# Optimization experiments

Measured on AMD Instinct MI355X. Metric: run time of the kernel, lower is better.

## Reference

```python
import math
import jax, jax.numpy as jnp
import numpy as np

L, B, T, D = 16, 2, 2048, 1024

def setup_inputs() -> dict:
    key = jax.random.key(0)
    ks = jax.random.split(key, 6)
    return {
        "layer_outputs": jax.random.normal(ks[0], (L, B, T, D), jnp.float32),
        # nn.Linear weights, init std=0.02 (torch Linear computes x @ W^T)
        "w_q": jax.random.normal(ks[1], (D, D), jnp.float32) * 0.02,
        "w_k": jax.random.normal(ks[2], (D, D), jnp.float32) * 0.02,
        # per-layer LayerScalingFactor scalars, init 1/L (jittered so grads are nontrivial)
        "ca_scales": 1.0 / L + jax.random.normal(ks[3], (L,), jnp.float32) * 0.01,
        # CrossLayerAttention temperature, init 1.0
        "ca_temp": jnp.ones((1,), jnp.float32),
        # output LayerNorm affine params
        "ln_w": jnp.ones((D,), jnp.float32) + jax.random.normal(ks[4], (D,), jnp.float32) * 0.01,
        "ln_b": jax.random.normal(ks[5], (D,), jnp.float32) * 0.01,
    }

def reference(layer_outputs, w_q, w_k, ca_scales, ca_temp, ln_w, ln_b):
    # AllLayerXSA.aggregate_layers, aggregation_mode='attention', num_heads=1 (H=1, so H*D == head_dim)
    l, b, t, d = layer_outputs.shape
    current = layer_outputs[-1]                                    # query = last layer, [B,T,D]
    q = jnp.einsum('btd,ed->bte', current, w_q)                    # query_proj (no bias)
    k = jnp.einsum('lbtd,ed->lbte', layer_outputs, w_k)            # key_proj over stacked layers
    # per-token scores over layers: [B,T,L]
    scores = jnp.einsum('btd,lbtd->btl', q, k) / (math.sqrt(d) * jnp.abs(ca_temp))
    attn = jax.nn.softmax(scores, axis=-1)
    # per-layer scaling + renormalization
    attn = attn * ca_scales                                        # broadcast over L
    attn = attn / (jnp.sum(attn, axis=-1, keepdims=True) + 1e-6)
    # accumulate: output += scale_l * attn_w_l * layer_l (scale applied a second time, as in source)
    out = jnp.einsum('btl,l,lbtd->btd', attn, ca_scales, layer_outputs)
    # output LayerNorm(head_dim), torch default eps=1e-5, biased variance
    mean = jnp.mean(out, axis=-1, keepdims=True)
    var = jnp.mean(jnp.square(out - mean), axis=-1, keepdims=True)
    out = (out - mean) / jnp.sqrt(var + 1e-5) * ln_w + ln_b
    return out
```

## Files before the change

### kernel.cpp

```cpp
#include <hip/hip_runtime.h>
#include <hip/hip_bf16.h>

#define LNUM 16
#define DDIM 1024
#define MTOK 4096

using bf16x8 = __attribute__((ext_vector_type(8))) short;
using s4v    = __attribute__((ext_vector_type(4))) short;
using f32x4  = __attribute__((ext_vector_type(4))) float;

__device__ inline short f2b(float f) {
  __hip_bfloat16 h = __float2bfloat16(f);
  union { __hip_bfloat16 h; short s; } u; u.h = h; return u.s;
}
__device__ inline float b2f(short s) {
  unsigned int u = ((unsigned int)(unsigned short)s) << 16;
  float f; __builtin_memcpy(&f, &u, 4); return f;
}
__device__ inline float bitsf(unsigned int u) {
  float f; __builtin_memcpy(&f, &u, 4); return f;
}

__global__ __launch_bounds__(256)
void pre_k(const float* __restrict__ wk, const float* __restrict__ wq,
           short* __restrict__ Wt,
           const float* __restrict__ xlast, short* __restrict__ xb)
{
  __shared__ short As[2][64 * 64];
  __shared__ short Bs[2][64 * 64];
  const int tid = threadIdx.x;

  if (blockIdx.x >= 256) {
    const size_t i = ((size_t)(blockIdx.x - 256) * 256 + tid) * 8;
    const float4 a = *reinterpret_cast<const float4*>(xlast + i);
    const float4 b = *reinterpret_cast<const float4*>(xlast + i + 4);
    bf16x8 v = { f2b(a.x), f2b(a.y), f2b(a.z), f2b(a.w),
                 f2b(b.x), f2b(b.y), f2b(b.z), f2b(b.w) };
    *reinterpret_cast<bf16x8*>(xb + i) = v;
    return;
  }

  const int lane = tid & 63;
  const int wave = tid >> 6;
  const int m0 = (blockIdx.x & 15) * 64;
  const int n0 = (blockIdx.x >> 4) * 64;
  const int wm = (wave >> 1) * 32;
  const int wn = (wave & 1) * 32;

  f32x4 acc[2][2] = {};
  const int col = tid & 63;
  const int kg  = tid >> 6;

  float ar[16], br[16];
  auto load = [&](int k0) {
    #pragma unroll
    for (int j = 0; j < 16; ++j) {
      const size_t k = (size_t)(k0 + kg * 16 + j);
      ar[j] = wk[k * 1024 + m0 + col];
      br[j] = wq[k * 1024 + n0 + col];
    }
  };
  auto store_lds = [&](int buf) {
    bf16x8 va0 = { f2b(ar[0]), f2b(ar[1]), f2b(ar[2]), f2b(ar[3]),
                   f2b(ar[4]), f2b(ar[5]), f2b(ar[6]), f2b(ar[7]) };
    bf16x8 va1 = { f2b(ar[8]), f2b(ar[9]), f2b(ar[10]), f2b(ar[11]),
                   f2b(ar[12]), f2b(ar[13]), f2b(ar[14]), f2b(ar[15]) };
    bf16x8 vb0 = { f2b(br[0]), f2b(br[1]), f2b(br[2]), f2b(br[3]),
                   f2b(br[4]), f2b(br[5]), f2b(br[6]), f2b(br[7]) };
    bf16x8 vb1 = { f2b(br[8]), f2b(br[9]), f2b(br[10]), f2b(br[11]),
                   f2b(br[12]), f2b(br[13]), f2b(br[14]), f2b(br[15]) };
    const int sw = (col & 7) << 4;
    const int b0 = (col * 128 + kg * 32) ^ sw;
    const int b1 = (col * 128 + kg * 32 + 16) ^ sw;
    char* pa = (char*)&As[buf][0];
    char* pb = (char*)&Bs[buf][0];
    *reinterpret_cast<bf16x8*>(pa + b0) = va0;
    *reinterpret_cast<bf16x8*>(pa + b1) = va1;
    *reinterpret_cast<bf16x8*>(pb + b0) = vb0;
    *reinterpret_cast<bf16x8*>(pb + b1) = vb1;
  };

  const int rl = lane & 15;
  const int hi = lane >> 4;
  auto compute = [&](int buf) {
    #pragma unroll
    for (int kk = 0; kk < 2; ++kk) {
      bf16x8 af[2], bfv[2];
      #pragma unroll
      for (int f = 0; f < 2; ++f) {
        const int row = wm + f * 16 + rl;
        af[f] = *reinterpret_cast<const bf16x8*>(
            (const char*)&As[buf][0] + ((row * 128 + kk * 64 + hi * 16) ^ ((row & 7) << 4)));
      }
      #pragma unroll
      for (int g = 0; g < 2; ++g) {
        const int row = wn + g * 16 + rl;
        bfv[g] = *reinterpret_cast<const bf16x8*>(
            (const char*)&Bs[buf][0] + ((row * 128 + kk * 64 + hi * 16) ^ ((row & 7) << 4)));
      }
      #pragma unroll
      for (int f = 0; f < 2; ++f)
        #pragma unroll
        for (int g = 0; g < 2; ++g)
          acc[f][g] = __builtin_amdgcn_mfma_f32_16x16x32_bf16(af[f], bfv[g], acc[f][g], 0, 0, 0);
    }
  };

  load(0);
  for (int t = 0; t < 16; ++t) {
    store_lds(t & 1);
    if (t < 15) load((t + 1) * 64);
    __syncthreads();
    compute(t & 1);
  }

  const int cl = lane & 15;
  const int rb = (lane >> 4) * 4;
  #pragma unroll
  for (int f = 0; f < 2; ++f)
    #pragma unroll
    for (int g = 0; g < 2; ++g) {
      size_t c = (size_t)(n0 + wn + g * 16 + cl);
      #pragma unroll
      for (int r = 0; r < 4; ++r) {
        size_t rr = (size_t)(m0 + wm + f * 16 + rb + r);
        Wt[rr * 1024 + c] = f2b(acc[f][g][r]);
      }
    }
}

__global__ __launch_bounds__(512)
void qk_gemm_k(const short* __restrict__ A, const short* __restrict__ B,
               short* __restrict__ C)
{
  __shared__ short As[2][128 * 64];
  __shared__ short Bs[2][128 * 64];
  const int tid  = threadIdx.x;
  const int lane = tid & 63;
  const int wave = tid >> 6;
  const int m0 = blockIdx.x * 128;
  const int n0 = blockIdx.y * 128;
  const int wm = (wave >> 2) * 64;
  const int wn = (wave & 3) * 32;

  f32x4 acc[4][2] = {};

  const int srow = lane >> 3;
  const int swz  = ((lane & 7) * 16) ^ (srow << 4);

  auto stage = [&](int buf, int k0) {
    #pragma unroll
    for (int c = 0; c < 2; ++c) {
      const int ch = wave * 2 + c;
      const int r  = ch * 8 + srow;
      const short* ga = A + (size_t)(m0 + r) * 1024 + k0 + (swz >> 1);
      __builtin_amdgcn_global_load_lds(
          (const __attribute__((address_space(1))) void*)ga,
          (__attribute__((address_space(3))) void*)&As[buf][ch * 512], 16, 0, 0);
      const short* gb = B + (size_t)(n0 + r) * 1024 + k0 + (swz >> 1);
      __builtin_amdgcn_global_load_lds(
          (const __attribute__((address_space(1))) void*)gb,
          (__attribute__((address_space(3))) void*)&Bs[buf][ch * 512], 16, 0, 0);
    }
  };

  const int rl = lane & 15;
  const int hi = lane >> 4;
  auto compute = [&](int buf) {
    #pragma unroll
    for (int kk = 0; kk < 2; ++kk) {
      bf16x8 af[4], bfv[2];
      #pragma unroll
      for (int i = 0; i < 4; ++i) {
        const int row = wm + i * 16 + rl;
        af[i] = *reinterpret_cast<const bf16x8*>(
            (const char*)&As[buf][0] + ((row * 128 + kk * 64 + hi * 16) ^ ((row & 7) << 4)));
      }
      #pragma unroll
      for (int g = 0; g < 2; ++g) {
        const int row = wn + g * 16 + rl;
        bfv[g] = *reinterpret_cast<const bf16x8*>(
            (const char*)&Bs[buf][0] + ((row * 128 + kk * 64 + hi * 16) ^ ((row & 7) << 4)));
      }
      #pragma unroll
      for (int i = 0; i < 4; ++i)
        #pragma unroll
        for (int g = 0; g < 2; ++g)
          acc[i][g] = __builtin_amdgcn_mfma_f32_16x16x32_bf16(af[i], bfv[g], acc[i][g], 0, 0, 0);
    }
  };

  stage(0, 0);
  __syncthreads();
  int buf = 0;
  for (int t = 0; t < 16; ++t) {
    if (t < 15) stage(buf ^ 1, (t + 1) * 64);
    compute(buf);
    __syncthreads();
    buf ^= 1;
  }

  const int cl = lane & 15;
  const int rb = (lane >> 4) * 4;
  #pragma unroll
  for (int i = 0; i < 4; ++i)
    #pragma unroll
    for (int g = 0; g < 2; ++g) {
      size_t c = (size_t)(n0 + wn + g * 16 + cl);
      #pragma unroll
      for (int r = 0; r < 4; ++r) {
        size_t rr = (size_t)(m0 + wm + i * 16 + rb + r);
        C[rr * 1024 + c] = f2b(acc[i][g][r]);
      }
    }
}

__global__ __launch_bounds__(256)
void fused_k(const float* __restrict__ layers, const short* __restrict__ qk,
             const float* __restrict__ scales, const float* __restrict__ temp,
             const float* __restrict__ lnw, const float* __restrict__ lnb,
             float* __restrict__ out)
{
  const int p    = blockIdx.x;
  const int tid  = threadIdx.x;
  const int lane = tid & 63;
  const int wave = tid >> 6;

  __shared__ float s_scales[16];
  __shared__ float s_red[4][16];
  __shared__ float s_scores[16];
  __shared__ float s_mv[4][2];

  if (tid < 16) s_scales[tid] = scales[tid];

  const size_t base = (size_t)p * DDIM + (size_t)tid * 4;
  s4v qv = *reinterpret_cast<const s4v*>(qk + base);
  const float q0 = b2f(qv.x), q1 = b2f(qv.y), q2 = b2f(qv.z), q3 = b2f(qv.w);

  unsigned int xpA[16], xpB[16];
  float v[16];
  #pragma unroll
  for (int l = 0; l < 16; ++l) {
    const float4 xv = *reinterpret_cast<const float4*>(layers + (size_t)l * MTOK * DDIM + base);
    v[l] = q0 * xv.x + q1 * xv.y + q2 * xv.z + q3 * xv.w;
    xpA[l] = ((unsigned int)(unsigned short)f2b(xv.y) << 16) | (unsigned short)f2b(xv.x);
    xpB[l] = ((unsigned int)(unsigned short)f2b(xv.w) << 16) | (unsigned short)f2b(xv.z);
  }

  #pragma unroll
  for (int j = 0; j < 8; ++j) {
    const bool hi = (lane & 1);
    float send = hi ? v[j] : v[j + 8];
    float keep = hi ? v[j + 8] : v[j];
    v[j] = keep + __shfl_xor(send, 1, 64);
  }
  #pragma unroll
  for (int j = 0; j < 4; ++j) {
    const bool hi = (lane & 2);
    float send = hi ? v[j] : v[j + 4];
    float keep = hi ? v[j + 4] : v[j];
    v[j] = keep + __shfl_xor(send, 2, 64);
  }
  #pragma unroll
  for (int j = 0; j < 2; ++j) {
    const bool hi = (lane & 4);
    float send = hi ? v[j] : v[j + 2];
    float keep = hi ? v[j + 2] : v[j];
    v[j] = keep + __shfl_xor(send, 4, 64);
  }
  {
    const bool hi = (lane & 8);
    float send = hi ? v[0] : v[1];
    float keep = hi ? v[1] : v[0];
    v[0] = keep + __shfl_xor(send, 8, 64);
  }
  v[0] += __shfl_xor(v[0], 16, 64);
  v[0] += __shfl_xor(v[0], 32, 64);
  if (lane < 16) {
    int l = ((lane & 1) << 3) | ((lane & 2) << 1) | ((lane & 4) >> 1) | ((lane & 8) >> 3);
    s_red[wave][l] = v[0];
  }
  __syncthreads();
  if (tid < 16)
    s_scores[tid] = s_red[0][tid] + s_red[1][tid] + s_red[2][tid] + s_red[3][tid];
  __syncthreads();

  const float inv = 1.0f / (32.0f * fabsf(temp[0]));
  float sc[16];
  float mx = -1e30f;
  #pragma unroll
  for (int l = 0; l < 16; ++l) { sc[l] = s_scores[l] * inv; mx = fmaxf(mx, sc[l]); }
  float se = 0.f;
  #pragma unroll
  for (int l = 0; l < 16; ++l) { sc[l] = __expf(sc[l] - mx); se += sc[l]; }
  const float rse = 1.0f / se;
  float t2 = 0.f;
  #pragma unroll
  for (int l = 0; l < 16; ++l) { sc[l] = sc[l] * rse * s_scales[l]; t2 += sc[l]; }
  const float rden = 1.0f / (t2 + 1e-6f);
  #pragma unroll
  for (int l = 0; l < 16; ++l) sc[l] *= s_scales[l] * rden;

  float o0 = 0.f, o1 = 0.f, o2 = 0.f, o3 = 0.f;
  #pragma unroll
  for (int l = 0; l < 16; ++l) {
    const float c = sc[l];
    o0 += c * bitsf(xpA[l] << 16);
    o1 += c * bitsf(xpA[l] & 0xffff0000u);
    o2 += c * bitsf(xpB[l] << 16);
    o3 += c * bitsf(xpB[l] & 0xffff0000u);
  }

  float sm = o0 + o1 + o2 + o3;
  float sq = o0 * o0 + o1 * o1 + o2 * o2 + o3 * o3;
  #pragma unroll
  for (int off = 1; off < 64; off <<= 1) {
    sm += __shfl_xor(sm, off, 64);
    sq += __shfl_xor(sq, off, 64);
  }
  if (lane == 0) { s_mv[wave][0] = sm; s_mv[wave][1] = sq; }
  __syncthreads();
  const float tsm = s_mv[0][0] + s_mv[1][0] + s_mv[2][0] + s_mv[3][0];
  const float tsq = s_mv[0][1] + s_mv[1][1] + s_mv[2][1] + s_mv[3][1];
  const float mean = tsm * (1.0f / 1024.0f);
  const float varv = tsq * (1.0f / 1024.0f) - mean * mean;
  const float rstd = rsqrtf(varv + 1e-5f);

  const float4 lw = *reinterpret_cast<const float4*>(lnw + (size_t)tid * 4);
  const float4 lb = *reinterpret_cast<const float4*>(lnb + (size_t)tid * 4);
  float4 res;
  res.x = (o0 - mean) * rstd * lw.x + lb.x;
  res.y = (o1 - mean) * rstd * lw.y + lb.y;
  res.z = (o2 - mean) * rstd * lw.z + lb.z;
  res.w = (o3 - mean) * rstd * lw.w + lb.w;
  *reinterpret_cast<float4*>(out + base) = res;
}

extern "C" void kernel_launch(void* const* d_in, const int* in_sizes, int n_in,
                              void* d_out, int out_size, void* d_ws, size_t ws_size,
                              hipStream_t stream)
{
  const float* layers = (const float*)d_in[0];
  const float* wq     = (const float*)d_in[1];
  const float* wk     = (const float*)d_in[2];
  const float* scales = (const float*)d_in[3];
  const float* temp   = (const float*)d_in[4];
  const float* lnw    = (const float*)d_in[5];
  const float* lnb    = (const float*)d_in[6];
  float* out = (float*)d_out;

  short* xb_ws = (short*)d_ws;
  short* wt_ws = xb_ws + (size_t)MTOK * DDIM;
  short* qk_ws = wt_ws + (size_t)DDIM * DDIM;

  const float* xlast = layers + (size_t)(LNUM - 1) * MTOK * DDIM;

  pre_k<<<dim3(256 + MTOK * DDIM / 2048), dim3(256), 0, stream>>>(wk, wq, wt_ws, xlast, xb_ws);
  qk_gemm_k<<<dim3(32, 8), dim3(512), 0, stream>>>(xb_ws, wt_ws, qk_ws);
  fused_k<<<dim3(MTOK), dim3(256), 0, stream>>>(layers, qk_ws, scales, temp, lnw, lnb, out);
}
```

Before: 92.80 us.

## Merge three kernels into one persistent kernel with software grid barriers

Replaces the weight-product, QK GEMM and fused attention/LayerNorm kernels with one 256-block persistent kernel that runs each phase in turn, separated by atomic-counter grid barriers. The x_last bf16 conversion is folded into the weight-GEMM phase, and the final phase processes 16 tokens per block, two at a time. This removes launch gaps and tail effects between kernels. In exchange it adds a hipMemsetAsync, spin-wait barriers that assume all 256 blocks are co-resident, and fewer resident threads for the memory-bound final phase, which may reduce latency hiding.

```diff
diff --git a/kernel.cpp b/kernel.cpp
--- a/kernel.cpp
+++ b/kernel.cpp
@@ -4,6 +4,7 @@
 #define LNUM 16
 #define DDIM 1024
 #define MTOK 4096
+#define NBLK 256
 
 using bf16x8 = __attribute__((ext_vector_type(8))) short;
 using s4v    = __attribute__((ext_vector_type(4))) short;
@@ -21,319 +22,321 @@
   float f; __builtin_memcpy(&f, &u, 4); return f;
 }
 
-__global__ __launch_bounds__(256)
-void pre_k(const float* __restrict__ wk, const float* __restrict__ wq,
-           short* __restrict__ Wt,
-           const float* __restrict__ xlast, short* __restrict__ xb)
-{
-  __shared__ short As[2][64 * 64];
-  __shared__ short Bs[2][64 * 64];
-  const int tid = threadIdx.x;
-
-  if (blockIdx.x >= 256) {
-    const size_t i = ((size_t)(blockIdx.x - 256) * 256 + tid) * 8;
-    const float4 a = *reinterpret_cast<const float4*>(xlast + i);
-    const float4 b = *reinterpret_cast<const float4*>(xlast + i + 4);
-    bf16x8 v = { f2b(a.x), f2b(a.y), f2b(a.z), f2b(a.w),
-                 f2b(b.x), f2b(b.y), f2b(b.z), f2b(b.w) };
-    *reinterpret_cast<bf16x8*>(xb + i) = v;
-    return;
-  }
-
-  const int lane = tid & 63;
-  const int wave = tid >> 6;
-  const int m0 = (blockIdx.x & 15) * 64;
-  const int n0 = (blockIdx.x >> 4) * 64;
-  const int wm = (wave >> 1) * 32;
-  const int wn = (wave & 1) * 32;
-
-  f32x4 acc[2][2] = {};
-  const int col = tid & 63;
-  const int kg  = tid >> 6;
-
-  float ar[16], br[16];
-  auto load = [&](int k0) {
-    #pragma unroll
-    for (int j = 0; j < 16; ++j) {
-      const size_t k = (size_t)(k0 + kg * 16 + j);
-      ar[j] = wk[k * 1024 + m0 + col];
-      br[j] = wq[k * 1024 + n0 + col];
-    }
-  };
-  auto store_lds = [&](int buf) {
-    bf16x8 va0 = { f2b(ar[0]), f2b(ar[1]), f2b(ar[2]), f2b(ar[3]),
-                   f2b(ar[4]), f2b(ar[5]), f2b(ar[6]), f2b(ar[7]) };
-    bf16x8 va1 = { f2b(ar[8]), f2b(ar[9]), f2b(ar[10]), f2b(ar[11]),
-                   f2b(ar[12]), f2b(ar[13]), f2b(ar[14]), f2b(ar[15]) };
-    bf16x8 vb0 = { f2b(br[0]), f2b(br[1]), f2b(br[2]), f2b(br[3]),
-                   f2b(br[4]), f2b(br[5]), f2b(br[6]), f2b(br[7]) };
-    bf16x8 vb1 = { f2b(br[8]), f2b(br[9]), f2b(br[10]), f2b(br[11]),
-                   f2b(br[12]), f2b(br[13]), f2b(br[14]), f2b(br[15]) };
-    const int sw = (col & 7) << 4;
-    const int b0 = (col * 128 + kg * 32) ^ sw;
-    const int b1 = (col * 128 + kg * 32 + 16) ^ sw;
-    char* pa = (char*)&As[buf][0];
-    char* pb = (char*)&Bs[buf][0];
-    *reinterpret_cast<bf16x8*>(pa + b0) = va0;
-    *reinterpret_cast<bf16x8*>(pa + b1) = va1;
-    *reinterpret_cast<bf16x8*>(pb + b0) = vb0;
-    *reinterpret_cast<bf16x8*>(pb + b1) = vb1;
-  };
-
-  const int rl = lane & 15;
-  const int hi = lane >> 4;
-  auto compute = [&](int buf) {
-    #pragma unroll
-    for (int kk = 0; kk < 2; ++kk) {
-      bf16x8 af[2], bfv[2];
-      #pragma unroll
-      for (int f = 0; f < 2; ++f) {
-        const int row = wm + f * 16 + rl;
-        af[f] = *reinterpret_cast<const bf16x8*>(
-            (const char*)&As[buf][0] + ((row * 128 + kk * 64 + hi * 16) ^ ((row & 7) << 4)));
-      }
-      #pragma unroll
-      for (int g = 0; g < 2; ++g) {
-        const int row = wn + g * 16 + rl;
-        bfv[g] = *reinterpret_cast<const bf16x8*>(
-            (const char*)&Bs[buf][0] + ((row * 128 + kk * 64 + hi * 16) ^ ((row & 7) << 4)));
-      }
-      #pragma unroll
-      for (int f = 0; f < 2; ++f)
-        #pragma unroll
-        for (int g = 0; g < 2; ++g)
-          acc[f][g] = __builtin_amdgcn_mfma_f32_16x16x32_bf16(af[f], bfv[g], acc[f][g], 0, 0, 0);
-    }
-  };
-
-  load(0);
-  for (int t = 0; t < 16; ++t) {
-    store_lds(t & 1);
-    if (t < 15) load((t + 1) * 64);
-    __syncthreads();
-    compute(t & 1);
-  }
-
-  const int cl = lane & 15;
-  const int rb = (lane >> 4) * 4;
-  #pragma unroll
-  for (int f = 0; f < 2; ++f)
-    #pragma unroll
-    for (int g = 0; g < 2; ++g) {
-      size_t c = (size_t)(n0 + wn + g * 16 + cl);
-      #pragma unroll
-      for (int r = 0; r < 4; ++r) {
-        size_t rr = (size_t)(m0 + wm + f * 16 + rb + r);
-        Wt[rr * 1024 + c] = f2b(acc[f][g][r]);
-      }
-    }
-}
-
-__global__ __launch_bounds__(512)
-void qk_gemm_k(const short* __restrict__ A, const short* __restrict__ B,
-               short* __restrict__ C)
-{
-  __shared__ short As[2][128 * 64];
-  __shared__ short Bs[2][128 * 64];
-  const int tid  = threadIdx.x;
-  const int lane = tid & 63;
-  const int wave = tid >> 6;
-  const int m0 = blockIdx.x * 128;
-  const int n0 = blockIdx.y * 128;
-  const int wm = (wave >> 2) * 64;
-  const int wn = (wave & 3) * 32;
-
-  f32x4 acc[4][2] = {};
-
-  const int srow = lane >> 3;
-  const int swz  = ((lane & 7) * 16) ^ (srow << 4);
-
-  auto stage = [&](int buf, int k0) {
-    #pragma unroll
-    for (int c = 0; c < 2; ++c) {
-      const int ch = wave * 2 + c;
-      const int r  = ch * 8 + srow;
-      const short* ga = A + (size_t)(m0 + r) * 1024 + k0 + (swz >> 1);
-      __builtin_amdgcn_global_load_lds(
-          (const __attribute__((address_space(1))) void*)ga,
-          (__attribute__((address_space(3))) void*)&As[buf][ch * 512], 16, 0, 0);
-      const short* gb = B + (size_t)(n0 + r) * 1024 + k0 + (swz >> 1);
-      __builtin_amdgcn_global_load_lds(
-          (const __attribute__((address_space(1))) void*)gb,
-          (__attribute__((address_space(3))) void*)&Bs[buf][ch * 512], 16, 0, 0);
-    }
-  };
-
-  const int rl = lane & 15;
-  const int hi = lane >> 4;
-  auto compute = [&](int buf) {
-    #pragma unroll
-    for (int kk = 0; kk < 2; ++kk) {
-      bf16x8 af[4], bfv[2];
-      #pragma unroll
-      for (int i = 0; i < 4; ++i) {
-        const int row = wm + i * 16 + rl;
-        af[i] = *reinterpret_cast<const bf16x8*>(
-            (const char*)&As[buf][0] + ((row * 128 + kk * 64 + hi * 16) ^ ((row & 7) << 4)));
-      }
-      #pragma unroll
-      for (int g = 0; g < 2; ++g) {
-        const int row = wn + g * 16 + rl;
-        bfv[g] = *reinterpret_cast<const bf16x8*>(
-            (const char*)&Bs[buf][0] + ((row * 128 + kk * 64 + hi * 16) ^ ((row & 7) << 4)));
-      }
-      #pragma unroll
-      for (int i = 0; i < 4; ++i)
-        #pragma unroll
-        for (int g = 0; g < 2; ++g)
-          acc[i][g] = __builtin_amdgcn_mfma_f32_16x16x32_bf16(af[i], bfv[g], acc[i][g], 0, 0, 0);
-    }
-  };
-
-  stage(0, 0);
+__device__ inline void grid_barrier(unsigned int* cnt) {
   __syncthreads();
-  int buf = 0;
-  for (int t = 0; t < 16; ++t) {
-    if (t < 15) stage(buf ^ 1, (t + 1) * 64);
-    compute(buf);
-    __syncthreads();
-    buf ^= 1;
-  }
-
-  const int cl = lane & 15;
-  const int rb = (lane >> 4) * 4;
-  #pragma unroll
-  for (int i = 0; i < 4; ++i)
-    #pragma unroll
-    for (int g = 0; g < 2; ++g) {
-      size_t c = (size_t)(n0 + wn + g * 16 + cl);
-      #pragma unroll
-      for (int r = 0; r < 4; ++r) {
-        size_t rr = (size_t)(m0 + wm + i * 16 + rb + r);
-        C[rr * 1024 + c] = f2b(acc[i][g][r]);
-      }
-    }
-}
-
-__global__ __launch_bounds__(256)
-void fused_k(const float* __restrict__ layers, const short* __restrict__ qk,
-             const float* __restrict__ scales, const float* __restrict__ temp,
-             const float* __restrict__ lnw, const float* __restrict__ lnb,
-             float* __restrict__ out)
-{
-  const int p    = blockIdx.x;
-  const int tid  = threadIdx.x;
-  const int lane = tid & 63;
-  const int wave = tid >> 6;
-
-  __shared__ float s_scales[16];
-  __shared__ float s_red[4][16];
-  __shared__ float s_scores[16];
-  __shared__ float s_mv[4][2];
-
-  if (tid < 16) s_scales[tid] = scales[tid];
-
-  const size_t base = (size_t)p * DDIM + (size_t)tid * 4;
-  s4v qv = *reinterpret_cast<const s4v*>(qk + base);
-  const float q0 = b2f(qv.x), q1 = b2f(qv.y), q2 = b2f(qv.z), q3 = b2f(qv.w);
-
-  unsigned int xpA[16], xpB[16];
-  float v[16];
-  #pragma unroll
-  for (int l = 0; l < 16; ++l) {
-    const float4 xv = *reinterpret_cast<const float4*>(layers + (size_t)l * MTOK * DDIM + base);
-    v[l] = q0 * xv.x + q1 * xv.y + q2 * xv.z + q3 * xv.w;
-    xpA[l] = ((unsigned int)(unsigned short)f2b(xv.y) << 16) | (unsigned short)f2b(xv.x);
-    xpB[l] = ((unsigned int)(unsigned short)f2b(xv.w) << 16) | (unsigned short)f2b(xv.z);
-  }
-
-  #pragma unroll
-  for (int j = 0; j < 8; ++j) {
-    const bool hi = (lane & 1);
-    float send = hi ? v[j] : v[j + 8];
-    float keep = hi ? v[j + 8] : v[j];
-    v[j] = keep + __shfl_xor(send, 1, 64);
-  }
-  #pragma unroll
-  for (int j = 0; j < 4; ++j) {
-    const bool hi = (lane & 2);
-    float send = hi ? v[j] : v[j + 4];
-    float keep = hi ? v[j + 4] : v[j];
-    v[j] = keep + __shfl_xor(send, 2, 64);
-  }
-  #pragma unroll
-  for (int j = 0; j < 2; ++j) {
-    const bool hi = (lane & 4);
-    float send = hi ? v[j] : v[j + 2];
-    float keep = hi ? v[j + 2] : v[j];
-    v[j] = keep + __shfl_xor(send, 4, 64);
-  }
-  {
-    const bool hi = (lane & 8);
-    float send = hi ? v[0] : v[1];
-    float keep = hi ? v[1] : v[0];
-    v[0] = keep + __shfl_xor(send, 8, 64);
-  }
-  v[0] += __shfl_xor(v[0], 16, 64);
-  v[0] += __shfl_xor(v[0], 32, 64);
-  if (lane < 16) {
-    int l = ((lane & 1) << 3) | ((lane & 2) << 1) | ((lane & 4) >> 1) | ((lane & 8) >> 3);
-    s_red[wave][l] = v[0];
+  if (threadIdx.x == 0) {
+    __threadfence();
+    atomicAdd(cnt, 1u);
+    unsigned int spins = 0;
+    while (__hip_atomic_load(cnt, __ATOMIC_ACQUIRE, __HIP_MEMORY_SCOPE_AGENT) < NBLK
+           && spins < 10000000u) {
+      ++spins;
+      __builtin_amdgcn_s_sleep(2);
+    }
   }
   __syncthreads();
-  if (tid < 16)
-    s_scores[tid] = s_red[0][tid] + s_red[1][tid] + s_red[2][tid] + s_red[3][tid];
-  __syncthreads();
-
-  const float inv = 1.0f / (32.0f * fabsf(temp[0]));
-  float sc[16];
-  float mx = -1e30f;
-  #pragma unroll
-  for (int l = 0; l < 16; ++l) { sc[l] = s_scores[l] * inv; mx = fmaxf(mx, sc[l]); }
-  float se = 0.f;
-  #pragma unroll
-  for (int l = 0; l < 16; ++l) { sc[l] = __expf(sc[l] - mx); se += sc[l]; }
-  const float rse = 1.0f / se;
-  float t2 = 0.f;
-  #pragma unroll
-  for (int l = 0; l < 16; ++l) { sc[l] = sc[l] * rse * s_scales[l]; t2 += sc[l]; }
-  const float rden = 1.0f / (t2 + 1e-6f);
-  #pragma unroll
-  for (int l = 0; l < 16; ++l) sc[l] *= s_scales[l] * rden;
-
-  float o0 = 0.f, o1 = 0.f, o2 = 0.f, o3 = 0.f;
-  #pragma unroll
-  for (int l = 0; l < 16; ++l) {
-    const float c = sc[l];
-    o0 += c * bitsf(xpA[l] << 16);
-    o1 += c * bitsf(xpA[l] & 0xffff0000u);
-    o2 += c * bitsf(xpB[l] << 16);
-    o3 += c * bitsf(xpB[l] & 0xffff0000u);
+  __threadfence();
+}
+
+__global__ __launch_bounds__(512)
+void mega_k(const float* __restrict__ layers, const float* __restrict__ wq,
+            const float* __restrict__ wk, const float* __restrict__ scales,
+            const float* __restrict__ temp, const float* __restrict__ lnw,
+            const float* __restrict__ lnb, float* __restrict__ out,
+            short* __restrict__ xb, short* __restrict__ wt,
+            short* __restrict__ qk, unsigned int* __restrict__ bar)
+{
+  __shared__ short sA[2][128 * 64];
+  __shared__ short sB[2][128 * 64];
+  __shared__ float s_scales[16];
+  __shared__ float s_red[2][4][16];
+  __shared__ float s_scores[2][16];
+  __shared__ float s_mv[2][4][2];
+
+  const int bid = blockIdx.x;
+  const int tid = threadIdx.x;
+  const float* xlast = layers + (size_t)(LNUM - 1) * MTOK * DDIM;
+
+  if (tid < 16) s_scales[tid] = scales[tid];
+
+  {
+    const int lane = tid & 63;
+    const int wave = tid >> 6;
+    const int m0 = (bid & 15) * 64;
+    const int n0 = (bid >> 4) * 64;
+    const int wm = (wave >> 2) * 32;
+    const int wn = (wave & 3) * 16;
+    f32x4 acc[2] = {};
+    const int col = tid & 63;
+    const int kg  = tid >> 6;
+
+    float ar[8], br[8];
+    auto load = [&](int k0) {
+      #pragma unroll
+      for (int j = 0; j < 8; ++j) {
+        const size_t k = (size_t)(k0 + kg * 8 + j);
+        ar[j] = wk[k * 1024 + m0 + col];
+        br[j] = wq[k * 1024 + n0 + col];
+      }
+    };
+    auto store_lds = [&](int buf) {
+      bf16x8 va = { f2b(ar[0]), f2b(ar[1]), f2b(ar[2]), f2b(ar[3]),
+                    f2b(ar[4]), f2b(ar[5]), f2b(ar[6]), f2b(ar[7]) };
+      bf16x8 vb = { f2b(br[0]), f2b(br[1]), f2b(br[2]), f2b(br[3]),
+                    f2b(br[4]), f2b(br[5]), f2b(br[6]), f2b(br[7]) };
+      const int b0 = (col * 128 + kg * 16) ^ ((col & 7) << 4);
+      *reinterpret_cast<bf16x8*>((char*)&sA[buf][0] + b0) = va;
+      *reinterpret_cast<bf16x8*>((char*)&sB[buf][0] + b0) = vb;
+    };
+    const int rl = lane & 15;
+    const int hi = lane >> 4;
+    auto compute = [&](int buf) {
+      #pragma unroll
+      for (int kk = 0; kk < 2; ++kk) {
+        bf16x8 af[2], bf1;
+        #pragma unroll
+        for (int f = 0; f < 2; ++f) {
+          const int row = wm + f * 16 + rl;
+          af[f] = *reinterpret_cast<const bf16x8*>(
+              (const char*)&sA[buf][0] + ((row * 128 + kk * 64 + hi * 16) ^ ((row & 7) << 4)));
+        }
+        {
+          const int row = wn + rl;
+          bf1 = *reinterpret_cast<const bf16x8*>(
+              (const char*)&sB[buf][0] + ((row * 128 + kk * 64 + hi * 16) ^ ((row & 7) << 4)));
+        }
+        #pragma unroll
+        for (int f = 0; f < 2; ++f)
+          acc[f] = __builtin_amdgcn_mfma_f32_16x16x32_bf16(af[f], bf1, acc[f], 0, 0, 0);
+      }
+    };
+
+    load(0);
+    for (int t = 0; t < 16; ++t) {
+      store_lds(t & 1);
+      if (t < 15) load((t + 1) * 64);
+      if ((t & 3) == 0) {
+        const size_t ci = (size_t)bid * 16384 + (size_t)(t >> 2) * 4096 + (size_t)tid * 8;
+        const float4 a = *reinterpret_cast<const float4*>(xlast + ci);
+        const float4 b = *reinterpret_cast<const float4*>(xlast + ci + 4);
+        bf16x8 v = { f2b(a.x), f2b(a.y), f2b(a.z), f2b(a.w),
+                     f2b(b.x), f2b(b.y), f2b(b.z), f2b(b.w) };
+        *reinterpret_cast<bf16x8*>(xb + ci) = v;
+      }
+      __syncthreads();
+      compute(t & 1);
+      __syncthreads();
+    }
+
+    const int cl = lane & 15;
+    const int rb = (lane >> 4) * 4;
+    #pragma unroll
+    for (int f = 0; f < 2; ++f) {
+      const size_t ccol = (size_t)(n0 + wn + cl);
+      #pragma unroll
+      for (int r = 0; r < 4; ++r) {
+        const size_t rr = (size_t)(m0 + wm + f * 16 + rb + r);
+        wt[rr * 1024 + ccol] = f2b(acc[f][r]);
+      }
+    }
   }
 
-  float sm = o0 + o1 + o2 + o3;
-  float sq = o0 * o0 + o1 * o1 + o2 * o2 + o3 * o3;
-  #pragma unroll
-  for (int off = 1; off < 64; off <<= 1) {
-    sm += __shfl_xor(sm, off, 64);
-    sq += __shfl_xor(sq, off, 64);
+  grid_barrier(&bar[0]);
+
+  {
+    const int lane = tid & 63;
+    const int wave = tid >> 6;
+    const int m0 = (bid & 31) * 128;
+    const int n0 = (bid >> 5) * 128;
+    const int wm = (wave >> 2) * 64;
+    const int wn = (wave & 3) * 32;
+
+    f32x4 acc[4][2] = {};
+    const int srow = lane >> 3;
+    const int swz  = ((lane & 7) * 16) ^ (srow << 4);
+
+    auto stage = [&](int buf, int k0) {
+      #pragma unroll
+      for (int c = 0; c < 2; ++c) {
+        const int ch = wave * 2 + c;
+        const int r  = ch * 8 + srow;
+        const short* ga = xb + (size_t)(m0 + r) * 1024 + k0 + (swz >> 1);
+        __builtin_amdgcn_global_load_lds(
+            (const __attribute__((address_space(1))) void*)ga,
+            (__attribute__((address_space(3))) void*)&sA[buf][ch * 512], 16, 0, 0);
+        const short* gb = wt + (size_t)(n0 + r) * 1024 + k0 + (swz >> 1);
+        __builtin_amdgcn_global_load_lds(
+            (const __attribute__((address_space(1))) void*)gb,
+            (__attribute__((address_space(3))) void*)&sB[buf][ch * 512], 16, 0, 0);
+      }
+    };
+    const int rl = lane & 15;
+    const int hi = lane >> 4;
+    auto compute = [&](int buf) {
+      #pragma unroll
+      for (int kk = 0; kk < 2; ++kk) {
+        bf16x8 af[4], bfv[2];
+        #pragma unroll
+        for (int i = 0; i < 4; ++i) {
+          const int row = wm + i * 16 + rl;
+          af[i] = *reinterpret_cast<const bf16x8*>(
+              (const char*)&sA[buf][0] + ((row * 128 + kk * 64 + hi * 16) ^ ((row & 7) << 4)));
+        }
+        #pragma unroll
+        for (int g = 0; g < 2; ++g) {
+          const int row = wn + g * 16 + rl;
+          bfv[g] = *reinterpret_cast<const bf16x8*>(
+              (const char*)&sB[buf][0] + ((row * 128 + kk * 64 + hi * 16) ^ ((row & 7) << 4)));
+        }
+        #pragma unroll
+        for (int i = 0; i < 4; ++i)
+          #pragma unroll
+          for (int g = 0; g < 2; ++g)
+            acc[i][g] = __builtin_amdgcn_mfma_f32_16x16x32_bf16(af[i], bfv[g], acc[i][g], 0, 0, 0);
+      }
+    };
+
+    stage(0, 0);
+    __syncthreads();
+    int buf = 0;
+    for (int t = 0; t < 16; ++t) {
+      if (t < 15) stage(buf ^ 1, (t + 1) * 64);
+      compute(buf);
+      __syncthreads();
+      buf ^= 1;
+    }
+
+    const int cl = lane & 15;
+    const int rb = (lane >> 4) * 4;
+    #pragma unroll
+    for (int i = 0; i < 4; ++i)
+      #pragma unroll
+      for (int g = 0; g < 2; ++g) {
+        const size_t c = (size_t)(n0 + wn + g * 16 + cl);
+        #pragma unroll
+        for (int r = 0; r < 4; ++r) {
+          const size_t rr = (size_t)(m0 + wm + i * 16 + rb + r);
+          qk[rr * 1024 + c] = f2b(acc[i][g][r]);
+        }
+      }
   }
-  if (lane == 0) { s_mv[wave][0] = sm; s_mv[wave][1] = sq; }
-  __syncthreads();
-  const float tsm = s_mv[0][0] + s_mv[1][0] + s_mv[2][0] + s_mv[3][0];
-  const float tsq = s_mv[0][1] + s_mv[1][1] + s_mv[2][1] + s_mv[3][1];
-  const float mean = tsm * (1.0f / 1024.0f);
-  const float varv = tsq * (1.0f / 1024.0f) - mean * mean;
-  const float rstd = rsqrtf(varv + 1e-5f);
-
-  const float4 lw = *reinterpret_cast<const float4*>(lnw + (size_t)tid * 4);
-  const float4 lb = *reinterpret_cast<const float4*>(lnb + (size_t)tid * 4);
-  float4 res;
-  res.x = (o0 - mean) * rstd * lw.x + lb.x;
-  res.y = (o1 - mean) * rstd * lw.y + lb.y;
-  res.z = (o2 - mean) * rstd * lw.z + lb.z;
-  res.w = (o3 - mean) * rstd * lw.w + lb.w;
-  *reinterpret_cast<float4*>(out + base) = res;
+
+  grid_barrier(&bar[1]);
+
+  {
+    const int lane = tid & 63;
+    const int wv   = tid >> 6;
+    const int sub  = wv >> 2;
+    const int swv  = wv & 3;
+    const int stid = tid & 255;
+    const float invt = 1.0f / (32.0f * fabsf(temp[0]));
+
+    for (int it = 0; it < 16; it += 2) {
+      const int p = bid * 16 + it + sub;
+      const size_t base = (size_t)p * DDIM + (size_t)stid * 4;
+      const s4v qv = *reinterpret_cast<const s4v*>(qk + base);
+      const float q0 = b2f(qv.x), q1 = b2f(qv.y), q2 = b2f(qv.z), q3 = b2f(qv.w);
+
+      unsigned int xpA[16], xpB[16];
+      float v[16];
+      #pragma unroll
+      for (int l = 0; l < 16; ++l) {
+        const float4 xv = *reinterpret_cast<const float4*>(layers + (size_t)l * MTOK * DDIM + base);
+        v[l] = q0 * xv.x + q1 * xv.y + q2 * xv.z + q3 * xv.w;
+        xpA[l] = ((unsigned int)(unsigned short)f2b(xv.y) << 16) | (unsigned short)f2b(xv.x);
+        xpB[l] = ((unsigned int)(unsigned short)f2b(xv.w) << 16) | (unsigned short)f2b(xv.z);
+      }
+
+      #pragma unroll
+      for (int j = 0; j < 8; ++j) {
+        const bool hi = (lane & 1);
+        float send = hi ? v[j] : v[j + 8];
+        float keep = hi ? v[j + 8] : v[j];
+        v[j] = keep + __shfl_xor(send, 1, 64);
+      }
+      #pragma unroll
+      for (int j = 0; j < 4; ++j) {
+        const bool hi = (lane & 2);
+        float send = hi ? v[j] : v[j + 4];
+        float keep = hi ? v[j + 4] : v[j];
+        v[j] = keep + __shfl_xor(send, 2, 64);
+      }
+      #pragma unroll
+      for (int j = 0; j < 2; ++j) {
+        const bool hi = (lane & 4);
+        float send = hi ? v[j] : v[j + 2];
+        float keep = hi ? v[j + 2] : v[j];
+        v[j] = keep + __shfl_xor(send, 4, 64);
+      }
+      {
+        const bool hi = (lane & 8);
+        float send = hi ? v[0] : v[1];
+        float keep = hi ? v[1] : v[0];
+        v[0] = keep + __shfl_xor(send, 8, 64);
+      }
+      v[0] += __shfl_xor(v[0], 16, 64);
+      v[0] += __shfl_xor(v[0], 32, 64);
+      if (lane < 16) {
+        int l = ((lane & 1) << 3) | ((lane & 2) << 1) | ((lane & 4) >> 1) | ((lane & 8) >> 3);
+        s_red[sub][swv][l] = v[0];
+      }
+      __syncthreads();
+      if (stid < 16)
+        s_scores[sub][stid] = s_red[sub][0][stid] + s_red[sub][1][stid]
+                            + s_red[sub][2][stid] + s_red[sub][3][stid];
+      __syncthreads();
+
+      float sc[16];
+      float mx = -1e30f;
+      #pragma unroll
+      for (int l = 0; l < 16; ++l) { sc[l] = s_scores[sub][l] * invt; mx = fmaxf(mx, sc[l]); }
+      float se = 0.f;
+      #pragma unroll
+      for (int l = 0; l < 16; ++l) { sc[l] = __expf(sc[l] - mx); se += sc[l]; }
+      const float rse = 1.0f / se;
+      float t2 = 0.f;
+      #pragma unroll
+      for (int l = 0; l < 16; ++l) { sc[l] = sc[l] * rse * s_scales[l]; t2 += sc[l]; }
+      const float rden = 1.0f / (t2 + 1e-6f);
+      #pragma unroll
+      for (int l = 0; l < 16; ++l) sc[l] *= s_scales[l] * rden;
+
+      float o0 = 0.f, o1 = 0.f, o2 = 0.f, o3 = 0.f;
+      #pragma unroll
+      for (int l = 0; l < 16; ++l) {
+        const float c = sc[l];
+        o0 += c * bitsf(xpA[l] << 16);
+        o1 += c * bitsf(xpA[l] & 0xffff0000u);
+        o2 += c * bitsf(xpB[l] << 16);
+        o3 += c * bitsf(xpB[l] & 0xffff0000u);
+      }
+
+      float sm = o0 + o1 + o2 + o3;
+      float sq = o0 * o0 + o1 * o1 + o2 * o2 + o3 * o3;
+      #pragma unroll
+      for (int off = 1; off < 64; off <<= 1) {
+        sm += __shfl_xor(sm, off, 64);
+        sq += __shfl_xor(sq, off, 64);
+      }
+      if (lane == 0) { s_mv[sub][swv][0] = sm; s_mv[sub][swv][1] = sq; }
+      __syncthreads();
+      const float tsm = s_mv[sub][0][0] + s_mv[sub][1][0] + s_mv[sub][2][0] + s_mv[sub][3][0];
+      const float tsq = s_mv[sub][0][1] + s_mv[sub][1][1] + s_mv[sub][2][1] + s_mv[sub][3][1];
+      const float mean = tsm * (1.0f / 1024.0f);
+      const float varv = tsq * (1.0f / 1024.0f) - mean * mean;
+      const float rstd = rsqrtf(varv + 1e-5f);
+
+      const float4 lw = *reinterpret_cast<const float4*>(lnw + (size_t)stid * 4);
+      const float4 lb = *reinterpret_cast<const float4*>(lnb + (size_t)stid * 4);
+      float4 res;
+      res.x = (o0 - mean) * rstd * lw.x + lb.x;
+      res.y = (o1 - mean) * rstd * lw.y + lb.y;
+      res.z = (o2 - mean) * rstd * lw.z + lb.z;
+      res.w = (o3 - mean) * rstd * lw.w + lb.w;
+      *reinterpret_cast<float4*>(out + base) = res;
+      __syncthreads();
+    }
+  }
 }
 
 extern "C" void kernel_launch(void* const* d_in, const int* in_sizes, int n_in,
@@ -352,10 +355,9 @@
   short* xb_ws = (short*)d_ws;
   short* wt_ws = xb_ws + (size_t)MTOK * DDIM;
   short* qk_ws = wt_ws + (size_t)DDIM * DDIM;
-
-  const float* xlast = layers + (size_t)(LNUM - 1) * MTOK * DDIM;
-
-  pre_k<<<dim3(256 + MTOK * DDIM / 2048), dim3(256), 0, stream>>>(wk, wq, wt_ws, xlast, xb_ws);
-  qk_gemm_k<<<dim3(32, 8), dim3(512), 0, stream>>>(xb_ws, wt_ws, qk_ws);
-  fused_k<<<dim3(MTOK), dim3(256), 0, stream>>>(layers, qk_ws, scales, temp, lnw, lnb, out);
-}
+  unsigned int* bar = (unsigned int*)((char*)d_ws + (20u << 20));
+
+  hipMemsetAsync(bar, 0, 8, stream);
+  mega_k<<<dim3(NBLK), dim3(512), 0, stream>>>(
+      layers, wq, wk, scales, temp, lnw, lnb, out, xb_ws, wt_ws, qk_ws, bar);
+}
```

New measurement: 203.1 us. 2.19x slower.

## Process two tokens per block, prefetching second token's layers during first's reductions

Applied to the files above, without the earlier changes.

The fused attention/LayerNorm kernel now handles two tokens per block with half as many blocks. The second token's 16 layer loads are issued right after the first token's loads, so their memory latency overlaps the first token's score reduction, softmax and LayerNorm. This aims to keep more bytes in flight per wave in a bandwidth-bound kernel. The cost is much higher register pressure (64 extra floats held for xr plus packed arrays), which may cut occupancy or cause spills, and there are fewer blocks.

```diff
diff --git a/kernel.cpp b/kernel.cpp
--- a/kernel.cpp
+++ b/kernel.cpp
@@ -216,12 +216,11 @@
 }
 
 __global__ __launch_bounds__(256)
-void fused_k(const float* __restrict__ layers, const short* __restrict__ qk,
-             const float* __restrict__ scales, const float* __restrict__ temp,
-             const float* __restrict__ lnw, const float* __restrict__ lnb,
-             float* __restrict__ out)
+void fused2_k(const float* __restrict__ layers, const short* __restrict__ qk,
+              const float* __restrict__ scales, const float* __restrict__ temp,
+              const float* __restrict__ lnw, const float* __restrict__ lnb,
+              float* __restrict__ out)
 {
-  const int p    = blockIdx.x;
   const int tid  = threadIdx.x;
   const int lane = tid & 63;
   const int wave = tid >> 6;
@@ -233,107 +232,217 @@
 
   if (tid < 16) s_scales[tid] = scales[tid];
 
-  const size_t base = (size_t)p * DDIM + (size_t)tid * 4;
-  s4v qv = *reinterpret_cast<const s4v*>(qk + base);
-  const float q0 = b2f(qv.x), q1 = b2f(qv.y), q2 = b2f(qv.z), q3 = b2f(qv.w);
-
-  unsigned int xpA[16], xpB[16];
-  float v[16];
+  const size_t base0 = (size_t)(blockIdx.x * 2) * DDIM + (size_t)tid * 4;
+  const size_t base1 = base0 + DDIM;
+
+  const s4v qv0 = *reinterpret_cast<const s4v*>(qk + base0);
+  const float a_q0 = b2f(qv0.x), a_q1 = b2f(qv0.y), a_q2 = b2f(qv0.z), a_q3 = b2f(qv0.w);
+
+  unsigned int xpA0[16], xpB0[16];
+  float v0[16];
   #pragma unroll
   for (int l = 0; l < 16; ++l) {
-    const float4 xv = *reinterpret_cast<const float4*>(layers + (size_t)l * MTOK * DDIM + base);
-    v[l] = q0 * xv.x + q1 * xv.y + q2 * xv.z + q3 * xv.w;
-    xpA[l] = ((unsigned int)(unsigned short)f2b(xv.y) << 16) | (unsigned short)f2b(xv.x);
-    xpB[l] = ((unsigned int)(unsigned short)f2b(xv.w) << 16) | (unsigned short)f2b(xv.z);
-  }
+    const float4 xv = *reinterpret_cast<const float4*>(layers + (size_t)l * MTOK * DDIM + base0);
+    v0[l] = a_q0 * xv.x + a_q1 * xv.y + a_q2 * xv.z + a_q3 * xv.w;
+    xpA0[l] = ((unsigned int)(unsigned short)f2b(xv.y) << 16) | (unsigned short)f2b(xv.x);
+    xpB0[l] = ((unsigned int)(unsigned short)f2b(xv.w) << 16) | (unsigned short)f2b(xv.z);
+  }
+
+  const s4v qv1 = *reinterpret_cast<const s4v*>(qk + base1);
+  float4 xr[16];
+  #pragma unroll
+  for (int l = 0; l < 16; ++l)
+    xr[l] = *reinterpret_cast<const float4*>(layers + (size_t)l * MTOK * DDIM + base1);
 
   #pragma unroll
   for (int j = 0; j < 8; ++j) {
     const bool hi = (lane & 1);
-    float send = hi ? v[j] : v[j + 8];
-    float keep = hi ? v[j + 8] : v[j];
-    v[j] = keep + __shfl_xor(send, 1, 64);
+    float send = hi ? v0[j] : v0[j + 8];
+    float keep = hi ? v0[j + 8] : v0[j];
+    v0[j] = keep + __shfl_xor(send, 1, 64);
   }
   #pragma unroll
   for (int j = 0; j < 4; ++j) {
     const bool hi = (lane & 2);
-    float send = hi ? v[j] : v[j + 4];
-    float keep = hi ? v[j + 4] : v[j];
-    v[j] = keep + __shfl_xor(send, 2, 64);
+    float send = hi ? v0[j] : v0[j + 4];
+    float keep = hi ? v0[j + 4] : v0[j];
+    v0[j] = keep + __shfl_xor(send, 2, 64);
   }
   #pragma unroll
   for (int j = 0; j < 2; ++j) {
     const bool hi = (lane & 4);
-    float send = hi ? v[j] : v[j + 2];
-    float keep = hi ? v[j + 2] : v[j];
-    v[j] = keep + __shfl_xor(send, 4, 64);
+    float send = hi ? v0[j] : v0[j + 2];
+    float keep = hi ? v0[j + 2] : v0[j];
+    v0[j] = keep + __shfl_xor(send, 4, 64);
   }
   {
     const bool hi = (lane & 8);
-    float send = hi ? v[0] : v[1];
-    float keep = hi ? v[1] : v[0];
-    v[0] = keep + __shfl_xor(send, 8, 64);
-  }
-  v[0] += __shfl_xor(v[0], 16, 64);
-  v[0] += __shfl_xor(v[0], 32, 64);
+    float send = hi ? v0[0] : v0[1];
+    float keep = hi ? v0[1] : v0[0];
+    v0[0] = keep + __shfl_xor(send, 8, 64);
+  }
+  v0[0] += __shfl_xor(v0[0], 16, 64);
+  v0[0] += __shfl_xor(v0[0], 32, 64);
   if (lane < 16) {
     int l = ((lane & 1) << 3) | ((lane & 2) << 1) | ((lane & 4) >> 1) | ((lane & 8) >> 3);
-    s_red[wave][l] = v[0];
+    s_red[wave][l] = v0[0];
   }
   __syncthreads();
   if (tid < 16)
     s_scores[tid] = s_red[0][tid] + s_red[1][tid] + s_red[2][tid] + s_red[3][tid];
   __syncthreads();
 
-  const float inv = 1.0f / (32.0f * fabsf(temp[0]));
-  float sc[16];
-  float mx = -1e30f;
-  #pragma unroll
-  for (int l = 0; l < 16; ++l) { sc[l] = s_scores[l] * inv; mx = fmaxf(mx, sc[l]); }
-  float se = 0.f;
-  #pragma unroll
-  for (int l = 0; l < 16; ++l) { sc[l] = __expf(sc[l] - mx); se += sc[l]; }
-  const float rse = 1.0f / se;
-  float t2 = 0.f;
-  #pragma unroll
-  for (int l = 0; l < 16; ++l) { sc[l] = sc[l] * rse * s_scales[l]; t2 += sc[l]; }
-  const float rden = 1.0f / (t2 + 1e-6f);
-  #pragma unroll
-  for (int l = 0; l < 16; ++l) sc[l] *= s_scales[l] * rden;
-
-  float o0 = 0.f, o1 = 0.f, o2 = 0.f, o3 = 0.f;
+  const float b_q0 = b2f(qv1.x), b_q1 = b2f(qv1.y), b_q2 = b2f(qv1.z), b_q3 = b2f(qv1.w);
+  unsigned int xpA1[16], xpB1[16];
+  float v1[16];
   #pragma unroll
   for (int l = 0; l < 16; ++l) {
-    const float c = sc[l];
-    o0 += c * bitsf(xpA[l] << 16);
-    o1 += c * bitsf(xpA[l] & 0xffff0000u);
-    o2 += c * bitsf(xpB[l] << 16);
-    o3 += c * bitsf(xpB[l] & 0xffff0000u);
-  }
-
-  float sm = o0 + o1 + o2 + o3;
-  float sq = o0 * o0 + o1 * o1 + o2 * o2 + o3 * o3;
-  #pragma unroll
-  for (int off = 1; off < 64; off <<= 1) {
-    sm += __shfl_xor(sm, off, 64);
-    sq += __shfl_xor(sq, off, 64);
-  }
-  if (lane == 0) { s_mv[wave][0] = sm; s_mv[wave][1] = sq; }
-  __syncthreads();
-  const float tsm = s_mv[0][0] + s_mv[1][0] + s_mv[2][0] + s_mv[3][0];
-  const float tsq = s_mv[0][1] + s_mv[1][1] + s_mv[2][1] + s_mv[3][1];
-  const float mean = tsm * (1.0f / 1024.0f);
-  const float varv = tsq * (1.0f / 1024.0f) - mean * mean;
-  const float rstd = rsqrtf(varv + 1e-5f);
-
-  const float4 lw = *reinterpret_cast<const float4*>(lnw + (size_t)tid * 4);
-  const float4 lb = *reinterpret_cast<const float4*>(lnb + (size_t)tid * 4);
-  float4 res;
-  res.x = (o0 - mean) * rstd * lw.x + lb.x;
-  res.y = (o1 - mean) * rstd * lw.y + lb.y;
-  res.z = (o2 - mean) * rstd * lw.z + lb.z;
-  res.w = (o3 - mean) * rstd * lw.w + lb.w;
-  *reinterpret_cast<float4*>(out + base) = res;
+    v1[l] = b_q0 * xr[l].x + b_q1 * xr[l].y + b_q2 * xr[l].z + b_q3 * xr[l].w;
+    xpA1[l] = ((unsigned int)(unsigned short)f2b(xr[l].y) << 16) | (unsigned short)f2b(xr[l].x);
+    xpB1[l] = ((unsigned int)(unsigned short)f2b(xr[l].w) << 16) | (unsigned short)f2b(xr[l].z);
+  }
+
+  const float invt = 1.0f / (32.0f * fabsf(temp[0]));
+  {
+    float sc[16];
+    float mx = -1e30f;
+    #pragma unroll
+    for (int l = 0; l < 16; ++l) { sc[l] = s_scores[l] * invt; mx = fmaxf(mx, sc[l]); }
+    float se = 0.f;
+    #pragma unroll
+    for (int l = 0; l < 16; ++l) { sc[l] = __expf(sc[l] - mx); se += sc[l]; }
+    const float rse = 1.0f / se;
+    float t2 = 0.f;
+    #pragma unroll
+    for (int l = 0; l < 16; ++l) { sc[l] = sc[l] * rse * s_scales[l]; t2 += sc[l]; }
+    const float rden = 1.0f / (t2 + 1e-6f);
+    #pragma unroll
+    for (int l = 0; l < 16; ++l) sc[l] *= s_scales[l] * rden;
+
+    float o0 = 0.f, o1 = 0.f, o2 = 0.f, o3 = 0.f;
+    #pragma unroll
+    for (int l = 0; l < 16; ++l) {
+      const float c = sc[l];
+      o0 += c * bitsf(xpA0[l] << 16);
+      o1 += c * bitsf(xpA0[l] & 0xffff0000u);
+      o2 += c * bitsf(xpB0[l] << 16);
+      o3 += c * bitsf(xpB0[l] & 0xffff0000u);
+    }
+
+    float sm = o0 + o1 + o2 + o3;
+    float sq = o0 * o0 + o1 * o1 + o2 * o2 + o3 * o3;
+    #pragma unroll
+    for (int off = 1; off < 64; off <<= 1) {
+      sm += __shfl_xor(sm, off, 64);
+      sq += __shfl_xor(sq, off, 64);
+    }
+    if (lane == 0) { s_mv[wave][0] = sm; s_mv[wave][1] = sq; }
+    __syncthreads();
+    const float tsm = s_mv[0][0] + s_mv[1][0] + s_mv[2][0] + s_mv[3][0];
+    const float tsq = s_mv[0][1] + s_mv[1][1] + s_mv[2][1] + s_mv[3][1];
+    const float mean = tsm * (1.0f / 1024.0f);
+    const float varv = tsq * (1.0f / 1024.0f) - mean * mean;
+    const float rstd = rsqrtf(varv + 1e-5f);
+
+    const float4 lw = *reinterpret_cast<const float4*>(lnw + (size_t)tid * 4);
+    const float4 lb = *reinterpret_cast<const float4*>(lnb + (size_t)tid * 4);
+    float4 res;
+    res.x = (o0 - mean) * rstd * lw.x + lb.x;
+    res.y = (o1 - mean) * rstd * lw.y + lb.y;
+    res.z = (o2 - mean) * rstd * lw.z + lb.z;
+    res.w = (o3 - mean) * rstd * lw.w + lb.w;
+    *reinterpret_cast<float4*>(out + base0) = res;
+  }
+  __syncthreads();
+
+  #pragma unroll
+  for (int j = 0; j < 8; ++j) {
+    const bool hi = (lane & 1);
+    float send = hi ? v1[j] : v1[j + 8];
+    float keep = hi ? v1[j + 8] : v1[j];
+    v1[j] = keep + __shfl_xor(send, 1, 64);
+  }
+  #pragma unroll
+  for (int j = 0; j < 4; ++j) {
+    const bool hi = (lane & 2);
+    float send = hi ? v1[j] : v1[j + 4];
+    float keep = hi ? v1[j + 4] : v1[j];
+    v1[j] = keep + __shfl_xor(send, 2, 64);
+  }
+  #pragma unroll
+  for (int j = 0; j < 2; ++j) {
+    const bool hi = (lane & 4);
+    float send = hi ? v1[j] : v1[j + 2];
+    float keep = hi ? v1[j + 2] : v1[j];
+    v1[j] = keep + __shfl_xor(send, 4, 64);
+  }
+  {
+    const bool hi = (lane & 8);
+    float send = hi ? v1[0] : v1[1];
+    float keep = hi ? v1[1] : v1[0];
+    v1[0] = keep + __shfl_xor(send, 8, 64);
+  }
+  v1[0] += __shfl_xor(v1[0], 16, 64);
+  v1[0] += __shfl_xor(v1[0], 32, 64);
+  if (lane < 16) {
+    int l = ((lane & 1) << 3) | ((lane & 2) << 1) | ((lane & 4) >> 1) | ((lane & 8) >> 3);
+    s_red[wave][l] = v1[0];
+  }
+  __syncthreads();
+  if (tid < 16)
+    s_scores[tid] = s_red[0][tid] + s_red[1][tid] + s_red[2][tid] + s_red[3][tid];
+  __syncthreads();
+
+  {
+    float sc[16];
+    float mx = -1e30f;
+    #pragma unroll
+    for (int l = 0; l < 16; ++l) { sc[l] = s_scores[l] * invt; mx = fmaxf(mx, sc[l]); }
+    float se = 0.f;
+    #pragma unroll
+    for (int l = 0; l < 16; ++l) { sc[l] = __expf(sc[l] - mx); se += sc[l]; }
+    const float rse = 1.0f / se;
+    float t2 = 0.f;
+    #pragma unroll
+    for (int l = 0; l < 16; ++l) { sc[l] = sc[l] * rse * s_scales[l]; t2 += sc[l]; }
+    const float rden = 1.0f / (t2 + 1e-6f);
+    #pragma unroll
+    for (int l = 0; l < 16; ++l) sc[l] *= s_scales[l] * rden;
+
+    float o0 = 0.f, o1 = 0.f, o2 = 0.f, o3 = 0.f;
+    #pragma unroll
+    for (int l = 0; l < 16; ++l) {
+      const float c = sc[l];
+      o0 += c * bitsf(xpA1[l] << 16);
+      o1 += c * bitsf(xpA1[l] & 0xffff0000u);
+      o2 += c * bitsf(xpB1[l] << 16);
+      o3 += c * bitsf(xpB1[l] & 0xffff0000u);
+    }
+
+    float sm = o0 + o1 + o2 + o3;
+    float sq = o0 * o0 + o1 * o1 + o2 * o2 + o3 * o3;
+    #pragma unroll
+    for (int off = 1; off < 64; off <<= 1) {
+      sm += __shfl_xor(sm, off, 64);
+      sq += __shfl_xor(sq, off, 64);
+    }
+    if (lane == 0) { s_mv[wave][0] = sm; s_mv[wave][1] = sq; }
+    __syncthreads();
+    const float tsm = s_mv[0][0] + s_mv[1][0] + s_mv[2][0] + s_mv[3][0];
+    const float tsq = s_mv[0][1] + s_mv[1][1] + s_mv[2][1] + s_mv[3][1];
+    const float mean = tsm * (1.0f / 1024.0f);
+    const float varv = tsq * (1.0f / 1024.0f) - mean * mean;
+    const float rstd = rsqrtf(varv + 1e-5f);
+
+    const float4 lw = *reinterpret_cast<const float4*>(lnw + (size_t)tid * 4);
+    const float4 lb = *reinterpret_cast<const float4*>(lnb + (size_t)tid * 4);
+    float4 res;
+    res.x = (o0 - mean) * rstd * lw.x + lb.x;
+    res.y = (o1 - mean) * rstd * lw.y + lb.y;
+    res.z = (o2 - mean) * rstd * lw.z + lb.z;
+    res.w = (o3 - mean) * rstd * lw.w + lb.w;
+    *reinterpret_cast<float4*>(out + base1) = res;
+  }
 }
 
 extern "C" void kernel_launch(void* const* d_in, const int* in_sizes, int n_in,
@@ -357,5 +466,5 @@
 
   pre_k<<<dim3(256 + MTOK * DDIM / 2048), dim3(256), 0, stream>>>(wk, wq, wt_ws, xlast, xb_ws);
   qk_gemm_k<<<dim3(32, 8), dim3(512), 0, stream>>>(xb_ws, wt_ws, qk_ws);
-  fused_k<<<dim3(MTOK), dim3(256), 0, stream>>>(layers, qk_ws, scales, temp, lnw, lnb, out);
-}
+  fused2_k<<<dim3(MTOK / 2), dim3(256), 0, stream>>>(layers, qk_ws, scales, temp, lnw, lnb, out);
+}
```

Measured after the change: 92.86 us. Within noise of the previous version (+0.1%).
